# Performance work log

Measured on AMD Instinct MI355X. Metric: run time of the kernel, lower is better.

Reference implementation:

```python
import jax, jax.numpy as jnp
jax.config.update("jax_enable_x64", True)
import numpy as np

BATCH, N = 8192, 4096
EPS = 1e-6
NR_ITERS = 5  # Newton-Raphson iterations in the gate circuit


def setup_inputs() -> dict:
    key = jax.random.key(0)
    x = jax.random.normal(key, (BATCH, N), dtype=jnp.float32)
    return {"x": x}


def reference(x):
    # Faithful numeric emulation of the bit-pulse FP64 gate circuit.
    # The original encodes each scalar as 32 bit-pulses, widens to FP64,
    # and runs the exact arithmetic below on FP64 values, then narrows
    # back to FP32. We operate on the decoded floats directly.
    x64 = x.astype(jnp.float64)                      # FP32ToFP64Converter
    mean = jnp.mean(x64, axis=-1, keepdims=True)     # sum via FP64 adders / N
    c = x64 - mean                                   # x + (-mean) via sign NOT + adder
    var = jnp.mean(c * c, axis=-1, keepdims=True)    # FP64 squares, summed, / N
    vpe = var + EPS
    # rsqrt via Newton-Raphson, seeded with y0 = 1/(var+eps) (FP64 divider)
    y = 1.0 / vpe
    for _ in range(NR_ITERS):
        y = 0.5 * y * (3.0 - vpe * (y * y))
    out = c * y                                      # normalize
    return out.astype(jnp.float32)                   # FP64ToFP32Converter
```

## Files before the change

### kernel.cpp

```cpp
#include <hip/hip_runtime.h>


#define LN_BATCH   8192
#define LN_N       4096
#define LN_THREADS 256
#define LN_WAVES   4
#define LN_F4PT    4
#define LN_EPS     1e-6

typedef float vfloat4 __attribute__((ext_vector_type(4)));

__device__ __forceinline__ double wave_allreduce_add(double s) {
#pragma unroll
    for (int off = 1; off < 64; off <<= 1)
        s += __shfl_xor(s, off, 64);
    return s;
}

__global__ __launch_bounds__(LN_THREADS, 8)
void spike_layernorm_kernel(const float* __restrict__ x, float* __restrict__ out) {
    const int wave = threadIdx.x >> 6;
    const int lane = threadIdx.x & 63;
    const int row  = blockIdx.x;

    __shared__ double red[2][LN_WAVES];

    const vfloat4* __restrict__ xr =
        reinterpret_cast<const vfloat4*>(x + (size_t)row * LN_N);
    vfloat4* __restrict__ orow =
        reinterpret_cast<vfloat4*>(out + (size_t)row * LN_N);

    const int base = wave * (LN_N / 4 / LN_WAVES) + lane;

    vfloat4 v[LN_F4PT];
#pragma unroll
    for (int i = 0; i < LN_F4PT; ++i)
        v[i] = __builtin_nontemporal_load(&xr[base + i * 64]);

    double s0 = 0.0, s1 = 0.0;
#pragma unroll
    for (int i = 0; i < LN_F4PT; ++i) {
        s0 += (double)v[i].x + (double)v[i].y;
        s1 += (double)v[i].z + (double)v[i].w;
    }
    double s = wave_allreduce_add(s0 + s1);
    if (lane == 0) red[0][wave] = s;
    __syncthreads();
    const double mean =
        ((red[0][0] + red[0][1]) + (red[0][2] + red[0][3])) * (1.0 / LN_N);

    double q0 = 0.0, q1 = 0.0;
#pragma unroll
    for (int i = 0; i < LN_F4PT; ++i) {
        double d;
        d = (double)v[i].x - mean; q0 += d * d;
        d = (double)v[i].y - mean; q1 += d * d;
        d = (double)v[i].z - mean; q0 += d * d;
        d = (double)v[i].w - mean; q1 += d * d;
    }
    double q = wave_allreduce_add(q0 + q1);
    if (lane == 0) red[1][wave] = q;
    __syncthreads();
    const double var =
        ((red[1][0] + red[1][1]) + (red[1][2] + red[1][3])) * (1.0 / LN_N);

    const double vpe = var + LN_EPS;
    double y = 1.0 / vpe;
#pragma unroll
    for (int it = 0; it < 5; ++it)
        y = 0.5 * y * (3.0 - vpe * (y * y));

#pragma unroll
    for (int i = 0; i < LN_F4PT; ++i) {
        vfloat4 o;
        o.x = (float)(((double)v[i].x - mean) * y);
        o.y = (float)(((double)v[i].y - mean) * y);
        o.z = (float)(((double)v[i].z - mean) * y);
        o.w = (float)(((double)v[i].w - mean) * y);
        __builtin_nontemporal_store(o, &orow[base + i * 64]);
    }
}

extern "C" void kernel_launch(void* const* d_in, const int* in_sizes, int n_in,
                              void* d_out, int out_size, void* d_ws, size_t ws_size,
                              hipStream_t stream) {
    const float* x = (const float*)d_in[0];
    float* out = (float*)d_out;
    spike_layernorm_kernel<<<LN_BATCH, LN_THREADS, 0, stream>>>(x, out);
}
```

Baseline: 217.7 us.

## Process four rows per block and prefetch the next row into registers

The grid shrinks from one block per row to 2048 blocks, and each block loops over four rows strided by the grid size. While the current row's FP64 reductions and normalization run, the next row's vector loads are issued into a second register buffer, overlapping global memory latency with compute and barriers. This doubles the input register footprint, so the launch-bounds occupancy hint is lowered from 8 to 7. Fewer blocks also means less launch and tail work per row, at the cost of less parallelism to hide latency across blocks.

After: 217.1 us. Within noise of the previous version (-0.3%).

```diff
diff --git a/kernel.cpp b/kernel.cpp
--- a/kernel.cpp
+++ b/kernel.cpp
@@ -6,6 +6,8 @@
 #define LN_THREADS 256
 #define LN_WAVES   4
 #define LN_F4PT    4
+#define LN_GRID    2048
+#define LN_ROWS_PB (LN_BATCH / LN_GRID)
 #define LN_EPS     1e-6
 
 typedef float vfloat4 __attribute__((ext_vector_type(4)));
@@ -17,67 +19,85 @@
     return s;
 }
 
-__global__ __launch_bounds__(LN_THREADS, 8)
+__global__ __launch_bounds__(LN_THREADS, 7)
 void spike_layernorm_kernel(const float* __restrict__ x, float* __restrict__ out) {
     const int wave = threadIdx.x >> 6;
     const int lane = threadIdx.x & 63;
-    const int row  = blockIdx.x;
+    const int vbase = wave * (LN_N / 4 / LN_WAVES) + lane;
 
     __shared__ double red[2][LN_WAVES];
 
-    const vfloat4* __restrict__ xr =
-        reinterpret_cast<const vfloat4*>(x + (size_t)row * LN_N);
-    vfloat4* __restrict__ orow =
-        reinterpret_cast<vfloat4*>(out + (size_t)row * LN_N);
-
-    const int base = wave * (LN_N / 4 / LN_WAVES) + lane;
-
     vfloat4 v[LN_F4PT];
+    {
+        const vfloat4* __restrict__ xr =
+            reinterpret_cast<const vfloat4*>(x + (size_t)blockIdx.x * LN_N);
 #pragma unroll
-    for (int i = 0; i < LN_F4PT; ++i)
-        v[i] = __builtin_nontemporal_load(&xr[base + i * 64]);
-
-    double s0 = 0.0, s1 = 0.0;
-#pragma unroll
-    for (int i = 0; i < LN_F4PT; ++i) {
-        s0 += (double)v[i].x + (double)v[i].y;
-        s1 += (double)v[i].z + (double)v[i].w;
+        for (int i = 0; i < LN_F4PT; ++i)
+            v[i] = __builtin_nontemporal_load(&xr[vbase + i * 64]);
     }
-    double s = wave_allreduce_add(s0 + s1);
-    if (lane == 0) red[0][wave] = s;
-    __syncthreads();
-    const double mean =
-        ((red[0][0] + red[0][1]) + (red[0][2] + red[0][3])) * (1.0 / LN_N);
-
-    double q0 = 0.0, q1 = 0.0;
-#pragma unroll
-    for (int i = 0; i < LN_F4PT; ++i) {
-        double d;
-        d = (double)v[i].x - mean; q0 += d * d;
-        d = (double)v[i].y - mean; q1 += d * d;
-        d = (double)v[i].z - mean; q0 += d * d;
-        d = (double)v[i].w - mean; q1 += d * d;
-    }
-    double q = wave_allreduce_add(q0 + q1);
-    if (lane == 0) red[1][wave] = q;
-    __syncthreads();
-    const double var =
-        ((red[1][0] + red[1][1]) + (red[1][2] + red[1][3])) * (1.0 / LN_N);
-
-    const double vpe = var + LN_EPS;
-    double y = 1.0 / vpe;
-#pragma unroll
-    for (int it = 0; it < 5; ++it)
-        y = 0.5 * y * (3.0 - vpe * (y * y));
 
 #pragma unroll
-    for (int i = 0; i < LN_F4PT; ++i) {
-        vfloat4 o;
-        o.x = (float)(((double)v[i].x - mean) * y);
-        o.y = (float)(((double)v[i].y - mean) * y);
-        o.z = (float)(((double)v[i].z - mean) * y);
-        o.w = (float)(((double)v[i].w - mean) * y);
-        __builtin_nontemporal_store(o, &orow[base + i * 64]);
+    for (int it = 0; it < LN_ROWS_PB; ++it) {
+        const int r = blockIdx.x + it * LN_GRID;
+
+        vfloat4 w[LN_F4PT];
+        if (it + 1 < LN_ROWS_PB) {
+            const vfloat4* __restrict__ xn =
+                reinterpret_cast<const vfloat4*>(x + (size_t)(r + LN_GRID) * LN_N);
+#pragma unroll
+            for (int i = 0; i < LN_F4PT; ++i)
+                w[i] = __builtin_nontemporal_load(&xn[vbase + i * 64]);
+        }
+
+        double s0 = 0.0, s1 = 0.0;
+#pragma unroll
+        for (int i = 0; i < LN_F4PT; ++i) {
+            s0 += (double)v[i].x + (double)v[i].y;
+            s1 += (double)v[i].z + (double)v[i].w;
+        }
+        double s = wave_allreduce_add(s0 + s1);
+        if (lane == 0) red[0][wave] = s;
+        __syncthreads();
+        const double mean =
+            ((red[0][0] + red[0][1]) + (red[0][2] + red[0][3])) * (1.0 / LN_N);
+
+        double q0 = 0.0, q1 = 0.0;
+#pragma unroll
+        for (int i = 0; i < LN_F4PT; ++i) {
+            double d;
+            d = (double)v[i].x - mean; q0 += d * d;
+            d = (double)v[i].y - mean; q1 += d * d;
+            d = (double)v[i].z - mean; q0 += d * d;
+            d = (double)v[i].w - mean; q1 += d * d;
+        }
+        double q = wave_allreduce_add(q0 + q1);
+        if (lane == 0) red[1][wave] = q;
+        __syncthreads();
+        const double var =
+            ((red[1][0] + red[1][1]) + (red[1][2] + red[1][3])) * (1.0 / LN_N);
+
+        const double vpe = var + LN_EPS;
+        double y = 1.0 / vpe;
+#pragma unroll
+        for (int nr = 0; nr < 5; ++nr)
+            y = 0.5 * y * (3.0 - vpe * (y * y));
+
+        vfloat4* __restrict__ orow =
+            reinterpret_cast<vfloat4*>(out + (size_t)r * LN_N);
+#pragma unroll
+        for (int i = 0; i < LN_F4PT; ++i) {
+            vfloat4 o;
+            o.x = (float)(((double)v[i].x - mean) * y);
+            o.y = (float)(((double)v[i].y - mean) * y);
+            o.z = (float)(((double)v[i].z - mean) * y);
+            o.w = (float)(((double)v[i].w - mean) * y);
+            __builtin_nontemporal_store(o, &orow[vbase + i * 64]);
+        }
+
+        if (it + 1 < LN_ROWS_PB) {
+#pragma unroll
+            for (int i = 0; i < LN_F4PT; ++i) v[i] = w[i];
+        }
     }
 }
 
@@ -86,5 +106,5 @@
                               hipStream_t stream) {
     const float* x = (const float*)d_in[0];
     float* out = (float*)d_out;
-    spike_layernorm_kernel<<<LN_BATCH, LN_THREADS, 0, stream>>>(x, out);
+    spike_layernorm_kernel<<<LN_GRID, LN_THREADS, 0, stream>>>(x, out);
 }
```

## Make layernorm persistent with double-buffered LDS prefetch of next row

Applied to the files above, without the earlier changes.

Launches a fixed grid of 1024 blocks that each process 8 rows. The next row is prefetched into a double-buffered shared-memory staging area via direct global-to-LDS loads while the current row is reduced and normalized. Manual vmcnt waits and raw barriers replace __syncthreads. This is meant to hide global load latency that the one-row-per-block design exposed, at the cost of 32KB LDS per block, lower occupancy, and fragile hand-counted wait values.

Measured after the change: 232.9 us. 1.07x slower.

```diff
diff --git a/kernel.cpp b/kernel.cpp
--- a/kernel.cpp
+++ b/kernel.cpp
@@ -5,7 +5,8 @@
 #define LN_N       4096
 #define LN_THREADS 256
 #define LN_WAVES   4
-#define LN_F4PT    4
+#define LN_GRID    1024
+#define LN_ROWS_PB (LN_BATCH / LN_GRID)
 #define LN_EPS     1e-6
 
 typedef float vfloat4 __attribute__((ext_vector_type(4)));
@@ -17,67 +18,95 @@
     return s;
 }
 
-__global__ __launch_bounds__(LN_THREADS, 8)
+__global__ __launch_bounds__(LN_THREADS)
 void spike_layernorm_kernel(const float* __restrict__ x, float* __restrict__ out) {
     const int wave = threadIdx.x >> 6;
     const int lane = threadIdx.x & 63;
-    const int row  = blockIdx.x;
 
-    __shared__ double red[2][LN_WAVES];
+    __shared__ float buf[2][LN_N];
+    __shared__ double red[2][2][LN_WAVES];
 
-    const vfloat4* __restrict__ xr =
-        reinterpret_cast<const vfloat4*>(x + (size_t)row * LN_N);
-    vfloat4* __restrict__ orow =
-        reinterpret_cast<vfloat4*>(out + (size_t)row * LN_N);
+    const int fbase = wave * 1024 + lane * 4;
 
-    const int base = wave * (LN_N / 4 / LN_WAVES) + lane;
+    auto stage = [&](int b, int r) {
+        const float* g = x + (size_t)r * LN_N + fbase;
+#pragma unroll
+        for (int i = 0; i < 4; ++i) {
+            __builtin_amdgcn_global_load_lds(
+                (const __attribute__((address_space(1))) void*)(g + i * 256),
+                (__attribute__((address_space(3))) void*)(&buf[b][wave * 1024 + i * 256]),
+                16, 0, 0);
+        }
+    };
 
-    vfloat4 v[LN_F4PT];
-#pragma unroll
-    for (int i = 0; i < LN_F4PT; ++i)
-        v[i] = __builtin_nontemporal_load(&xr[base + i * 64]);
-
-    double s0 = 0.0, s1 = 0.0;
-#pragma unroll
-    for (int i = 0; i < LN_F4PT; ++i) {
-        s0 += (double)v[i].x + (double)v[i].y;
-        s1 += (double)v[i].z + (double)v[i].w;
-    }
-    double s = wave_allreduce_add(s0 + s1);
-    if (lane == 0) red[0][wave] = s;
-    __syncthreads();
-    const double mean =
-        ((red[0][0] + red[0][1]) + (red[0][2] + red[0][3])) * (1.0 / LN_N);
-
-    double q0 = 0.0, q1 = 0.0;
-#pragma unroll
-    for (int i = 0; i < LN_F4PT; ++i) {
-        double d;
-        d = (double)v[i].x - mean; q0 += d * d;
-        d = (double)v[i].y - mean; q1 += d * d;
-        d = (double)v[i].z - mean; q0 += d * d;
-        d = (double)v[i].w - mean; q1 += d * d;
-    }
-    double q = wave_allreduce_add(q0 + q1);
-    if (lane == 0) red[1][wave] = q;
-    __syncthreads();
-    const double var =
-        ((red[1][0] + red[1][1]) + (red[1][2] + red[1][3])) * (1.0 / LN_N);
-
-    const double vpe = var + LN_EPS;
-    double y = 1.0 / vpe;
-#pragma unroll
-    for (int it = 0; it < 5; ++it)
-        y = 0.5 * y * (3.0 - vpe * (y * y));
+    stage(0, blockIdx.x);
+    asm volatile("" ::: "memory");
 
 #pragma unroll
-    for (int i = 0; i < LN_F4PT; ++i) {
-        vfloat4 o;
-        o.x = (float)(((double)v[i].x - mean) * y);
-        o.y = (float)(((double)v[i].y - mean) * y);
-        o.z = (float)(((double)v[i].z - mean) * y);
-        o.w = (float)(((double)v[i].w - mean) * y);
-        __builtin_nontemporal_store(o, &orow[base + i * 64]);
+    for (int it = 0; it < LN_ROWS_PB; ++it) {
+        const int r = blockIdx.x + it * LN_GRID;
+        const int p = it & 1;
+
+        if (it + 1 < LN_ROWS_PB)
+            stage(p ^ 1, r + LN_GRID);
+
+        if (it == 0)
+            asm volatile("s_waitcnt vmcnt(4)" ::: "memory");
+        else if (it == LN_ROWS_PB - 1)
+            asm volatile("s_waitcnt vmcnt(0)" ::: "memory");
+        else
+            asm volatile("s_waitcnt vmcnt(8)" ::: "memory");
+
+        vfloat4 v[4];
+#pragma unroll
+        for (int i = 0; i < 4; ++i)
+            v[i] = *reinterpret_cast<const vfloat4*>(&buf[p][fbase + i * 256]);
+
+        double s0 = 0.0, s1 = 0.0;
+#pragma unroll
+        for (int i = 0; i < 4; ++i) {
+            s0 += (double)v[i].x + (double)v[i].y;
+            s1 += (double)v[i].z + (double)v[i].w;
+        }
+        double s = wave_allreduce_add(s0 + s1);
+        if (lane == 0) red[p][0][wave] = s;
+        asm volatile("s_waitcnt lgkmcnt(0)" ::: "memory");
+        __builtin_amdgcn_s_barrier();
+        const double mean =
+            ((red[p][0][0] + red[p][0][1]) + (red[p][0][2] + red[p][0][3])) * (1.0 / LN_N);
+
+        double q0 = 0.0, q1 = 0.0;
+#pragma unroll
+        for (int i = 0; i < 4; ++i) {
+            double d;
+            d = (double)v[i].x - mean; q0 += d * d;
+            d = (double)v[i].y - mean; q1 += d * d;
+            d = (double)v[i].z - mean; q0 += d * d;
+            d = (double)v[i].w - mean; q1 += d * d;
+        }
+        double q = wave_allreduce_add(q0 + q1);
+        if (lane == 0) red[p][1][wave] = q;
+        asm volatile("s_waitcnt lgkmcnt(0)" ::: "memory");
+        __builtin_amdgcn_s_barrier();
+        const double var =
+            ((red[p][1][0] + red[p][1][1]) + (red[p][1][2] + red[p][1][3])) * (1.0 / LN_N);
+
+        const double vpe = var + LN_EPS;
+        double y = 1.0 / vpe;
+#pragma unroll
+        for (int nr = 0; nr < 5; ++nr)
+            y = 0.5 * y * (3.0 - vpe * (y * y));
+
+        float* __restrict__ orow = out + (size_t)r * LN_N + fbase;
+#pragma unroll
+        for (int i = 0; i < 4; ++i) {
+            vfloat4 o;
+            o.x = (float)(((double)v[i].x - mean) * y);
+            o.y = (float)(((double)v[i].y - mean) * y);
+            o.z = (float)(((double)v[i].z - mean) * y);
+            o.w = (float)(((double)v[i].w - mean) * y);
+            __builtin_nontemporal_store(o, reinterpret_cast<vfloat4*>(orow + i * 256));
+        }
     }
 }
 
@@ -86,5 +115,5 @@
                               hipStream_t stream) {
     const float* x = (const float*)d_in[0];
     float* out = (float*)d_out;
-    spike_layernorm_kernel<<<LN_BATCH, LN_THREADS, 0, stream>>>(x, out);
+    spike_layernorm_kernel<<<LN_GRID, LN_THREADS, 0, stream>>>(x, out);
 }
```
